# Optimization experiments

Measured on AMD Instinct MI355X. Metric: run time of the kernel, lower is better.

The kernel has to match this reference:

```python
import jax, jax.numpy as jnp
from jax import lax
import numpy as np

DN = ('NCHW', 'OIHW', 'NCHW')


def _gaussian_kernel1d(ksize, sigma):
    # torchvision GaussianBlur kernel: linspace-centered, normalized pdf
    x = jnp.linspace(-(ksize - 1) * 0.5, (ksize - 1) * 0.5, ksize, dtype=jnp.float32)
    pdf = jnp.exp(-0.5 * (x / sigma) ** 2)
    return pdf / pdf.sum()


def gaussian_blur(x, ksize, sigma):
    # x: [B, 1, H, W]. Separable blur with reflect padding (== torchvision
    # GaussianBlur, whose 2D kernel is the outer product of the 1D kernel).
    k = _gaussian_kernel1d(ksize, sigma).astype(x.dtype)
    pad = ksize // 2
    xp = jnp.pad(x, ((0, 0), (0, 0), (pad, pad), (pad, pad)), mode='reflect')
    xh = lax.conv_general_dilated(xp, k.reshape(1, 1, ksize, 1), (1, 1), 'VALID',
                                  dimension_numbers=DN)
    return lax.conv_general_dilated(xh, k.reshape(1, 1, 1, ksize), (1, 1), 'VALID',
                                    dimension_numbers=DN)


def _batch_max_norm(x):
    m = jnp.max(x.reshape(x.shape[0], -1), axis=1).reshape(-1, 1, 1, 1)
    return x / m


def _batch_mean_norm(x):
    m = jnp.mean(x.reshape(x.shape[0], -1), axis=1).reshape(-1, 1, 1, 1)
    return x / m


def setup_inputs() -> dict:
    key = jax.random.key(0)
    k1, k2, k3 = jax.random.split(key, 3)
    B, C, H, W = 8, 19, 512, 512
    mask_parse = jax.random.uniform(k1, (B, C, H, W), dtype=jnp.float32)
    area_weights = jax.random.uniform(k2, (C,), dtype=jnp.float32)
    eye_shadows_weight = jax.random.uniform(k3, (1,), dtype=jnp.float32)
    return {"mask_parse": mask_parse, "area_weights": area_weights,
            "eye_shadows_weight": eye_shadows_weight}


def reference(mask_parse, area_weights, eye_shadows_weight):
    background_mask = mask_parse[:, 0:1]          # [B,1,H,W]

    def eye_weight_mask(eyes_mask):
        w = gaussian_blur(eyes_mask, 51, 15.0)
        w = w * (1.0 - eyes_mask) * (1.0 - background_mask)
        return _batch_max_norm(w)

    w_mask_l = eye_weight_mask(mask_parse[:, 4:5])
    w_mask_r = eye_weight_mask(mask_parse[:, 5:6])

    # sum_i mask_parse[:, i] * area_weights[i]
    mask = jnp.einsum('bchw,c->bhw', mask_parse, area_weights)[:, None]
    mask = mask + (w_mask_l + w_mask_r) * eye_shadows_weight
    mask = gaussian_blur(mask, 21, 2.0)
    return _batch_mean_norm(mask)
```

## Files before the change

### kernel.cpp

```cpp
#include <hip/hip_runtime.h>
#include <hip/hip_cooperative_groups.h>

namespace cg = cooperative_groups;

constexpr int B_ = 8, C_ = 19, H_ = 512, W_ = 512;
constexpr int HW_ = H_ * W_;
constexpr int NB = 512;
constexpr int NT = 512;
constexpr int QH = 128, QW = 128;

constexpr int LDSF    = 14880;
constexpr int A_OFF   = 14336;
constexpr int SAW_OFF = 14848;
constexpr int T2Q_OFF = 2944, WHQ_OFF = 3840;
constexpr int ST_S = 540;

constexpr long WS_BM   = 0;
constexpr long WS_EW   = 512;
constexpr long WS_ESUM = 1024;
constexpr long WS_DSG  = 4096;
constexpr long WS_T0   = WS_DSG + 16L * QH * QW;

__device__ __forceinline__ int refl(int i, int n) {
    i = (i < 0) ? -i : i;
    return (i >= n) ? (2 * n - 2 - i) : i;
}

template<int ND>
__device__ __forceinline__ void gauss_reg(float (&wkr)[ND], float sigma) {
    float s = 0.f;
#pragma unroll
    for (int d = 0; d < ND; ++d) {
        const float t = d / sigma;
        wkr[d] = expf(-0.5f * t * t);
        s += (d ? 2.f : 1.f) * wkr[d];
    }
    const float inv = 1.f / s;
#pragma unroll
    for (int d = 0; d < ND; ++d) wkr[d] *= inv;
}

__device__ __forceinline__ float aweight(int i, const float (&wkr)[11]) {
    float a = 0.f;
#pragma unroll
    for (int t = 0; t < 21; ++t) {
        const float k = wkr[(t < 10) ? (10 - t) : (t - 10)];
        const int o = i + 10 - t;
        if (o >= 0 && o < H_) a += k;
        if (i >= 1 && i <= 10 && t <= 10 - i) a += k;
        if (i >= 501 && i <= 510 && t >= 521 - i) a += k;
    }
    return a;
}

__device__ __forceinline__ void ds_tile(const float* __restrict__ mp,
                                        float* __restrict__ dsg, int tid, int vb)
{
    const int b = vb >> 6, eye = (vb >> 5) & 1, ht = vb & 31;
    const int z = eye * 8 + b;
    const float* sb = mp + ((long)b * C_ + 4 + eye) * HW_;
    const int q = tid >> 7, cg = tid & 127;
    const int fr = ht * 16 + q * 4;
    float s = 0.f;
#pragma unroll
    for (int r = 0; r < 4; ++r) {
        const float4 v = *(const float4*)(sb + (long)(fr + r) * W_ + 4 * cg);
        s += (v.x + v.y) + (v.z + v.w);
    }
    dsg[(long)z * (QH * QW) + (long)(ht * 4 + q) * QW + cg] = s * 0.0625f;
}

__device__ __forceinline__ void eye_q(const float* __restrict__ mp,
                                      const float* __restrict__ dsg,
                                      float* __restrict__ t0,
                                      float* __restrict__ blockmax,
                                      float* __restrict__ eyesumw,
                                      float* lds, int tid, int vb)
{
    float kq[8];
    gauss_reg(kq, 3.75f);
    const int b = vb >> 6, eye = (vb >> 5) & 1, ht = vb & 31;
    const int z = eye * 8 + b;
    const float* dz = dsg + (long)z * (QH * QW);

    __syncthreads();
    float* sgq = lds;
    for (int t = 0; t < 6; ++t) {
        const int e = tid + t * NT;
        if (e < 20 * 142) {
            const int r = e / 142, c = e - r * 142;
            sgq[r * 142 + c] = dz[(long)refl(ht * 4 - 8 + r, QH) * QW + refl(c - 7, QW)];
        }
    }
    __syncthreads();
    float* t2q = lds + T2Q_OFF;
    if (tid < 426) {
        const int g = tid / 142, c = tid - g * 142;
        float w[16];
#pragma unroll
        for (int s = 0; s < 16; ++s) w[s] = sgq[(2 * g + s) * 142 + c];
#pragma unroll
        for (int jr = 0; jr < 2; ++jr) {
            float a = 0.f;
#pragma unroll
            for (int d = 0; d < 15; ++d)
                a = fmaf(w[jr + d], kq[(d < 7) ? (7 - d) : (d - 7)], a);
            t2q[(2 * g + jr) * 142 + c] = a;
        }
    }
    __syncthreads();
    float* whq = lds + WHQ_OFF;
#pragma unroll
    for (int t = 0; t < 2; ++t) {
        const int e = tid + t * NT;
        if (e < 768) {
            const int s = e >> 7, c = e & 127;
            float a = 0.f;
#pragma unroll
            for (int d = 0; d < 15; ++d)
                a = fmaf(t2q[s * 142 + c + d], kq[(d < 7) ? (7 - d) : (d - 7)], a);
            whq[s * 130 + c + 1] = a;
        }
    }
    __syncthreads();
    if (tid < 6) {
        whq[tid * 130]       = whq[tid * 130 + 1];
        whq[tid * 130 + 129] = whq[tid * 130 + 128];
    }
    __syncthreads();
    if (ht == 0 && tid < 130)  whq[tid]           = whq[130 + tid];
    if (ht == 31 && tid < 130) whq[5 * 130 + tid] = whq[4 * 130 + tid];
    __syncthreads();

    const float* A = lds + A_OFF;
    const int c = tid;
    const int j = ((c + 2) >> 2) - 1;
    const float fc = 0.625f + 0.25f * (float)(c & 1) - 0.5f * (float)((c >> 1) & 1);
    float cv[6];
#pragma unroll
    for (int s = 0; s < 6; ++s) {
        const float a0 = whq[s * 130 + j + 1], a1 = whq[s * 130 + j + 2];
        cv[s] = fmaf(fc, a1 - a0, a0);
    }
    const float Aw = A[c];
    const long mbase = (long)b * C_ * HW_ + (long)(ht * 16) * W_ + c;
    const float* eyp = mp + mbase + (long)(4 + eye) * HW_;
    const float* bgp = mp + mbase;
    float* db = t0 + (long)z * HW_ + (long)(ht * 16) * W_ + c;
    float vmax = 0.f, vsum = 0.f;
#pragma unroll
    for (int o = 0; o < 16; ++o) {
        const int ls0 = (o + 2) >> 2;
        const float fr_ = 0.625f + 0.25f * (float)(o & 1) - 0.5f * (float)((o >> 1) & 1);
        const float wv = fmaf(fr_, cv[ls0 + 1] - cv[ls0], cv[ls0]);
        const float ey = eyp[(long)o * W_], bg = bgp[(long)o * W_];
        const float v = wv * (1.f - ey) * (1.f - bg);
        db[(long)o * W_] = v;
        vmax = fmaxf(vmax, v);
        vsum = fmaf(v, A[ht * 16 + o] * Aw, vsum);
    }
#pragma unroll
    for (int off = 32; off; off >>= 1) {
        vmax = fmaxf(vmax, __shfl_down(vmax, off));
        vsum += __shfl_down(vsum, off);
    }
    __syncthreads();
    if ((tid & 63) == 0) { lds[tid >> 6] = vmax; lds[8 + (tid >> 6)] = vsum; }
    __syncthreads();
    if (tid == 0) {
        float m = lds[0], s = lds[8];
        for (int i = 1; i < 8; ++i) { m = fmaxf(m, lds[i]); s += lds[8 + i]; }
        blockmax[z * 32 + ht] = m;
        eyesumw[z * 32 + ht] = s;
    }
}

__device__ __forceinline__ void einsum_part(const float* __restrict__ mp,
                                            float* __restrict__ t3,
                                            float* __restrict__ esum,
                                            float* lds, int tid, int vb)
{
    const float* A   = lds + A_OFF;
    const float* saw = lds + SAW_OFF;
    const int b = vb >> 6, chunk = vb & 63;
    float se = 0.f;
#pragma unroll
    for (int q = 0; q < 2; ++q) {
        const int p4 = chunk * 1024 + q * 512 + tid;
        const long p = (long)p4 * 4;
        const int h = (int)(p >> 9), w0 = (int)(p & 511);
        const float* mpb = mp + (long)b * C_ * HW_ + p;
        float4 acc = make_float4(0.f, 0.f, 0.f, 0.f);
#pragma unroll
        for (int c = 0; c < C_; ++c) {
            const float4 v = *(const float4*)(mpb + (long)c * HW_);
            const float a = saw[c];
            acc.x = fmaf(v.x, a, acc.x);
            acc.y = fmaf(v.y, a, acc.y);
            acc.z = fmaf(v.z, a, acc.z);
            acc.w = fmaf(v.w, a, acc.w);
        }
        *(float4*)(t3 + (long)b * HW_ + p) = acc;
        const float4 a4 = *(const float4*)(A + w0);
        se = fmaf(acc.x * a4.x + acc.y * a4.y + acc.z * a4.z + acc.w * a4.w,
                  A[h], se);
    }
#pragma unroll
    for (int off = 32; off; off >>= 1) se += __shfl_down(se, off);
    __syncthreads();
    if ((tid & 63) == 0) lds[tid >> 6] = se;
    __syncthreads();
    if (tid == 0) {
        float s = 0.f;
        for (int i = 0; i < 8; ++i) s += lds[i];
        esum[vb] = s;
    }
}

__device__ __forceinline__ void phaseB(const float* __restrict__ esw,
                                       const float* __restrict__ t0,
                                       const float* __restrict__ blockmax,
                                       const float* __restrict__ eyesumw,
                                       const float* __restrict__ esum,
                                       float* __restrict__ out,
                                       float* lds, int tid, int vb)
{
    float wkr[11];
    gauss_reg(wkr, 2.f);
    const int b = vb >> 6, tile6 = vb & 63, hb = tile6 * 8;

    float mxL = blockmax[b * 32], mxR = blockmax[(8 + b) * 32];
    float SeL = 0.f, SeR = 0.f, Se = 0.f;
    for (int i = 0; i < 32; ++i) {
        mxL = fmaxf(mxL, blockmax[b * 32 + i]);
        mxR = fmaxf(mxR, blockmax[(8 + b) * 32 + i]);
        SeL += eyesumw[b * 32 + i];
        SeR += eyesumw[(8 + b) * 32 + i];
    }
    for (int i = 0; i < 64; ++i) Se += esum[b * 64 + i];
    const float e = esw[0];
    const float sl = e / mxL, sr = e / mxR;
    const float scale = (float)HW_ / (Se + sl * SeL + sr * SeR);

    const float* t1 = t0 + (long)b * HW_;
    const float* t2 = t0 + (long)(8 + b) * HW_;
    const float* t3 = t0 + (long)(16 + b) * HW_;

    const int c = tid;
    float win[28];
#pragma unroll
    for (int i = 0; i < 28; ++i) {
        const long off = (long)refl(hb - 10 + i, H_) * W_ + c;
        win[i] = fmaf(t1[off], sl, fmaf(t2[off], sr, t3[off]));
    }
    float hv[8];
#pragma unroll
    for (int j = 0; j < 8; ++j) {
        float a = 0.f;
#pragma unroll
        for (int k = 0; k < 21; ++k)
            a = fmaf(win[j + k], wkr[(k < 10) ? (10 - k) : (k - 10)], a);
        hv[j] = a;
    }
    __syncthreads();
    float* st = lds;
#pragma unroll
    for (int j = 0; j < 8; ++j) st[j * ST_S + 12 + c] = hv[j];
    __syncthreads();
    if (tid < 224) {
        const int r = tid / 28, q = tid - r * 28;
        float* srow = st + r * ST_S;
        if (q < 12) srow[11 - q] = srow[13 + q];
        else { const int cc = q - 12; srow[524 + cc] = srow[522 - cc]; }
    }
    __syncthreads();
    {
        const int r = tid >> 6, g = tid & 63, c0 = g * 8;
        const float* srow = st + r * ST_S;
        float wn[32];
#pragma unroll
        for (int m = 0; m < 8; ++m) {
            const float4 v = *(const float4*)(srow + c0 + 4 * m);
            wn[4*m] = v.x; wn[4*m+1] = v.y; wn[4*m+2] = v.z; wn[4*m+3] = v.w;
        }
        float oo[8];
#pragma unroll
        for (int o = 0; o < 8; ++o) {
            float a = 0.f;
#pragma unroll
            for (int k = 0; k < 21; ++k)
                a = fmaf(wn[o + 2 + k], wkr[(k < 10) ? (10 - k) : (k - 10)], a);
            oo[o] = a * scale;
        }
        float* orow = out + (long)b * HW_ + (long)(hb + r) * W_ + c0;
        *(float4*)(orow)     = make_float4(oo[0], oo[1], oo[2], oo[3]);
        *(float4*)(orow + 4) = make_float4(oo[4], oo[5], oo[6], oo[7]);
    }
}

__global__ void __launch_bounds__(NT, 4)
mega_kern(const float* __restrict__ mp, const float* __restrict__ aw,
          const float* __restrict__ esw, float* __restrict__ out,
          float* __restrict__ ws)
{
    cg::grid_group grid = cg::this_grid();
    __shared__ __align__(16) float lds[LDSF];
    const int tid = threadIdx.x, bid = blockIdx.x;
    const int vb = (bid & 7) * 64 + (bid >> 3);
    float* blockmax = ws + WS_BM;
    float* eyesumw  = ws + WS_EW;
    float* esum     = ws + WS_ESUM;
    float* dsg      = ws + WS_DSG;
    float* t0       = ws + WS_T0;
    float* t3       = t0 + 16L * HW_;

    {
        float w21[11];
        gauss_reg(w21, 2.f);
        lds[A_OFF + tid] = aweight(tid, w21);
    }
    if (tid < C_) lds[SAW_OFF + tid] = aw[tid];
    __syncthreads();

    ds_tile(mp, dsg, tid, vb);
    grid.sync();

    if (bid & 1) {
        einsum_part(mp, t3, esum, lds, tid, vb);
        eye_q(mp, dsg, t0, blockmax, eyesumw, lds, tid, vb);
    } else {
        eye_q(mp, dsg, t0, blockmax, eyesumw, lds, tid, vb);
        einsum_part(mp, t3, esum, lds, tid, vb);
    }
    grid.sync();

    phaseB(esw, t0, blockmax, eyesumw, esum, out, lds, tid, vb);
}

__global__ void __launch_bounds__(NT)
fb_P0_kern(const float* __restrict__ mp, float* __restrict__ ws)
{
    const int bid = blockIdx.x;
    const int vb = (bid & 7) * 64 + (bid >> 3);
    ds_tile(mp, ws + WS_DSG, threadIdx.x, vb);
}

__global__ void __launch_bounds__(NT)
fb_P1_kern(const float* __restrict__ mp, const float* __restrict__ aw,
           float* __restrict__ ws)
{
    __shared__ __align__(16) float lds[LDSF];
    const int tid = threadIdx.x, bid = blockIdx.x;
    const int vb = (bid & 7) * 64 + (bid >> 3);
    float* t0 = ws + WS_T0;
    {
        float w21[11];
        gauss_reg(w21, 2.f);
        lds[A_OFF + tid] = aweight(tid, w21);
    }
    if (tid < C_) lds[SAW_OFF + tid] = aw[tid];
    __syncthreads();
    if (bid & 1) {
        einsum_part(mp, t0 + 16L * HW_, ws + WS_ESUM, lds, tid, vb);
        eye_q(mp, ws + WS_DSG, t0, ws + WS_BM, ws + WS_EW, lds, tid, vb);
    } else {
        eye_q(mp, ws + WS_DSG, t0, ws + WS_BM, ws + WS_EW, lds, tid, vb);
        einsum_part(mp, t0 + 16L * HW_, ws + WS_ESUM, lds, tid, vb);
    }
}

__global__ void __launch_bounds__(NT)
fb_P2_kern(const float* __restrict__ esw, float* __restrict__ out,
           float* __restrict__ ws)
{
    __shared__ __align__(16) float lds[LDSF];
    const int tid = threadIdx.x, bid = blockIdx.x;
    const int vb = (bid & 7) * 64 + (bid >> 3);
    phaseB(esw, ws + WS_T0, ws + WS_BM, ws + WS_EW, ws + WS_ESUM,
           out, lds, tid, vb);
}

extern "C" void kernel_launch(void* const* d_in, const int* in_sizes, int n_in,
                              void* d_out, int out_size, void* d_ws, size_t ws_size,
                              hipStream_t stream)
{
    const float* mp  = (const float*)d_in[0];
    const float* aw  = (const float*)d_in[1];
    const float* esw = (const float*)d_in[2];
    float* out = (float*)d_out;
    float* wsf = (float*)d_ws;

    int coop = 0, nb = 0;
    hipDeviceGetAttribute(&coop, hipDeviceAttributeCooperativeLaunch, 0);
    hipOccupancyMaxActiveBlocksPerMultiprocessor(&nb, (const void*)mega_kern, NT, 0);

    if (coop && nb >= 2) {
        void* args[] = { (void*)&mp, (void*)&aw, (void*)&esw, (void*)&out, (void*)&wsf };
        hipLaunchCooperativeKernel((void*)mega_kern, dim3(NB), dim3(NT), args, 0, stream);
    } else {
        fb_P0_kern<<<NB, NT, 0, stream>>>(mp, wsf);
        fb_P1_kern<<<NB, NT, 0, stream>>>(mp, aw, wsf);
        fb_P2_kern<<<NB, NT, 0, stream>>>(esw, out, wsf);
    }
}
```

Measured before the change: 53.57 us.

## Replace cooperative mega-kernel with three regular launches and split einsum blocks

Drops the cooperative launch and its two grid-wide syncs in favour of three ordinary kernel launches on one stream. Eye work and einsum work now run in separate blocks of one mixed 1536-block launch instead of being done in sequence by each block. Per-kernel LDS is cut so more blocks can be resident, and the einsum is split into 1024 half-size chunks with a matching change in the phase-B reduction. It also removes the per-call occupancy and attribute queries on the host, at the cost of two extra kernel launch overheads.

```diff
diff --git a/kernel.cpp b/kernel.cpp
--- a/kernel.cpp
+++ b/kernel.cpp
@@ -1,18 +1,12 @@
 #include <hip/hip_runtime.h>
-#include <hip/hip_cooperative_groups.h>
-
-namespace cg = cooperative_groups;
 
 constexpr int B_ = 8, C_ = 19, H_ = 512, W_ = 512;
 constexpr int HW_ = H_ * W_;
-constexpr int NB = 512;
 constexpr int NT = 512;
 constexpr int QH = 128, QW = 128;
 
-constexpr int LDSF    = 14880;
-constexpr int A_OFF   = 14336;
-constexpr int SAW_OFF = 14848;
-constexpr int T2Q_OFF = 2944, WHQ_OFF = 3840;
+constexpr int T2Q_OFF = 2944, WHQ_OFF = 3840, A_OFF = 4640, SAW_OFF = 5152;
+constexpr int K1_LDSF = 5184;
 constexpr int ST_S = 540;
 
 constexpr long WS_BM   = 0;
@@ -53,9 +47,12 @@
     return a;
 }
 
-__device__ __forceinline__ void ds_tile(const float* __restrict__ mp,
-                                        float* __restrict__ dsg, int tid, int vb)
-{
+__global__ void __launch_bounds__(NT)
+k0_ds(const float* __restrict__ mp, float* __restrict__ ws)
+{
+    float* dsg = ws + WS_DSG;
+    const int bid = blockIdx.x, tid = threadIdx.x;
+    const int vb = (bid & 7) * 64 + (bid >> 3);
     const int b = vb >> 6, eye = (vb >> 5) & 1, ht = vb & 31;
     const int z = eye * 8 + b;
     const float* sb = mp + ((long)b * C_ + 4 + eye) * HW_;
@@ -83,7 +80,6 @@
     const int z = eye * 8 + b;
     const float* dz = dsg + (long)z * (QH * QW);
 
-    __syncthreads();
     float* sgq = lds;
     for (int t = 0; t < 6; ++t) {
         const int e = tid + t * NT;
@@ -175,36 +171,31 @@
     }
 }
 
-__device__ __forceinline__ void einsum_part(const float* __restrict__ mp,
+__device__ __forceinline__ void einsum_half(const float* __restrict__ mp,
                                             float* __restrict__ t3,
                                             float* __restrict__ esum,
-                                            float* lds, int tid, int vb)
+                                            float* lds, int tid, int idx)
 {
     const float* A   = lds + A_OFF;
     const float* saw = lds + SAW_OFF;
-    const int b = vb >> 6, chunk = vb & 63;
-    float se = 0.f;
-#pragma unroll
-    for (int q = 0; q < 2; ++q) {
-        const int p4 = chunk * 1024 + q * 512 + tid;
-        const long p = (long)p4 * 4;
-        const int h = (int)(p >> 9), w0 = (int)(p & 511);
-        const float* mpb = mp + (long)b * C_ * HW_ + p;
-        float4 acc = make_float4(0.f, 0.f, 0.f, 0.f);
-#pragma unroll
-        for (int c = 0; c < C_; ++c) {
-            const float4 v = *(const float4*)(mpb + (long)c * HW_);
-            const float a = saw[c];
-            acc.x = fmaf(v.x, a, acc.x);
-            acc.y = fmaf(v.y, a, acc.y);
-            acc.z = fmaf(v.z, a, acc.z);
-            acc.w = fmaf(v.w, a, acc.w);
-        }
-        *(float4*)(t3 + (long)b * HW_ + p) = acc;
-        const float4 a4 = *(const float4*)(A + w0);
-        se = fmaf(acc.x * a4.x + acc.y * a4.y + acc.z * a4.z + acc.w * a4.w,
-                  A[h], se);
-    }
+    const int b = idx >> 7, ch = idx & 127;
+    const int p4 = ch * 512 + tid;
+    const long p = (long)p4 * 4;
+    const int h = (int)(p >> 9), w0 = (int)(p & 511);
+    const float* mpb = mp + (long)b * C_ * HW_ + p;
+    float4 acc = make_float4(0.f, 0.f, 0.f, 0.f);
+#pragma unroll
+    for (int c = 0; c < C_; ++c) {
+        const float4 v = *(const float4*)(mpb + (long)c * HW_);
+        const float a = saw[c];
+        acc.x = fmaf(v.x, a, acc.x);
+        acc.y = fmaf(v.y, a, acc.y);
+        acc.z = fmaf(v.z, a, acc.z);
+        acc.w = fmaf(v.w, a, acc.w);
+    }
+    *(float4*)(t3 + (long)b * HW_ + p) = acc;
+    const float4 a4 = *(const float4*)(A + w0);
+    float se = (acc.x * a4.x + acc.y * a4.y + acc.z * a4.z + acc.w * a4.w) * A[h];
 #pragma unroll
     for (int off = 32; off; off >>= 1) se += __shfl_down(se, off);
     __syncthreads();
@@ -213,18 +204,53 @@
     if (tid == 0) {
         float s = 0.f;
         for (int i = 0; i < 8; ++i) s += lds[i];
-        esum[vb] = s;
-    }
-}
-
-__device__ __forceinline__ void phaseB(const float* __restrict__ esw,
-                                       const float* __restrict__ t0,
-                                       const float* __restrict__ blockmax,
-                                       const float* __restrict__ eyesumw,
-                                       const float* __restrict__ esum,
-                                       float* __restrict__ out,
-                                       float* lds, int tid, int vb)
-{
+        esum[idx] = s;
+    }
+}
+
+__global__ void __launch_bounds__(NT, 8)
+k1_mix(const float* __restrict__ mp, const float* __restrict__ aw,
+       float* __restrict__ ws)
+{
+    __shared__ __align__(16) float lds[K1_LDSF];
+    const int tid = threadIdx.x, bid = blockIdx.x;
+    float* blockmax = ws + WS_BM;
+    float* eyesumw  = ws + WS_EW;
+    float* esum     = ws + WS_ESUM;
+    float* dsg      = ws + WS_DSG;
+    float* t0       = ws + WS_T0;
+    float* t3       = t0 + 16L * HW_;
+
+    {
+        float w21[11];
+        gauss_reg(w21, 2.f);
+        lds[A_OFF + tid] = aweight(tid, w21);
+    }
+    if (tid < C_) lds[SAW_OFF + tid] = aw[tid];
+    __syncthreads();
+
+    if (bid < 512) {
+        const int vb = (bid & 7) * 64 + (bid >> 3);
+        eye_q(mp, dsg, t0, blockmax, eyesumw, lds, tid, vb);
+    } else {
+        const int raw = bid - 512;
+        const int idx = (raw & 7) * 128 + (raw >> 3);
+        einsum_half(mp, t3, esum, lds, tid, idx);
+    }
+}
+
+__global__ void __launch_bounds__(NT, 4)
+k2_blur(const float* __restrict__ esw, float* __restrict__ out,
+        float* __restrict__ ws)
+{
+    __shared__ __align__(16) float lds[ST_S * 8 + 32];
+    const int tid = threadIdx.x, bid = blockIdx.x;
+    const int vb = (bid & 7) * 64 + (bid >> 3);
+    const float* blockmax = ws + WS_BM;
+    const float* eyesumw  = ws + WS_EW;
+    const float* esum     = ws + WS_ESUM;
+    const float* t0       = ws + WS_T0;
+
     float wkr[11];
     gauss_reg(wkr, 2.f);
     const int b = vb >> 6, tile6 = vb & 63, hb = tile6 * 8;
@@ -237,7 +263,7 @@
         SeL += eyesumw[b * 32 + i];
         SeR += eyesumw[(8 + b) * 32 + i];
     }
-    for (int i = 0; i < 64; ++i) Se += esum[b * 64 + i];
+    for (int i = 0; i < 128; ++i) Se += esum[b * 128 + i];
     const float e = esw[0];
     const float sl = e / mxL, sr = e / mxR;
     const float scale = (float)HW_ / (Se + sl * SeL + sr * SeR);
@@ -262,7 +288,6 @@
             a = fmaf(win[j + k], wkr[(k < 10) ? (10 - k) : (k - 10)], a);
         hv[j] = a;
     }
-    __syncthreads();
     float* st = lds;
 #pragma unroll
     for (int j = 0; j < 8; ++j) st[j * ST_S + 12 + c] = hv[j];
@@ -298,88 +323,6 @@
     }
 }
 
-__global__ void __launch_bounds__(NT, 4)
-mega_kern(const float* __restrict__ mp, const float* __restrict__ aw,
-          const float* __restrict__ esw, float* __restrict__ out,
-          float* __restrict__ ws)
-{
-    cg::grid_group grid = cg::this_grid();
-    __shared__ __align__(16) float lds[LDSF];
-    const int tid = threadIdx.x, bid = blockIdx.x;
-    const int vb = (bid & 7) * 64 + (bid >> 3);
-    float* blockmax = ws + WS_BM;
-    float* eyesumw  = ws + WS_EW;
-    float* esum     = ws + WS_ESUM;
-    float* dsg      = ws + WS_DSG;
-    float* t0       = ws + WS_T0;
-    float* t3       = t0 + 16L * HW_;
-
-    {
-        float w21[11];
-        gauss_reg(w21, 2.f);
-        lds[A_OFF + tid] = aweight(tid, w21);
-    }
-    if (tid < C_) lds[SAW_OFF + tid] = aw[tid];
-    __syncthreads();
-
-    ds_tile(mp, dsg, tid, vb);
-    grid.sync();
-
-    if (bid & 1) {
-        einsum_part(mp, t3, esum, lds, tid, vb);
-        eye_q(mp, dsg, t0, blockmax, eyesumw, lds, tid, vb);
-    } else {
-        eye_q(mp, dsg, t0, blockmax, eyesumw, lds, tid, vb);
-        einsum_part(mp, t3, esum, lds, tid, vb);
-    }
-    grid.sync();
-
-    phaseB(esw, t0, blockmax, eyesumw, esum, out, lds, tid, vb);
-}
-
-__global__ void __launch_bounds__(NT)
-fb_P0_kern(const float* __restrict__ mp, float* __restrict__ ws)
-{
-    const int bid = blockIdx.x;
-    const int vb = (bid & 7) * 64 + (bid >> 3);
-    ds_tile(mp, ws + WS_DSG, threadIdx.x, vb);
-}
-
-__global__ void __launch_bounds__(NT)
-fb_P1_kern(const float* __restrict__ mp, const float* __restrict__ aw,
-           float* __restrict__ ws)
-{
-    __shared__ __align__(16) float lds[LDSF];
-    const int tid = threadIdx.x, bid = blockIdx.x;
-    const int vb = (bid & 7) * 64 + (bid >> 3);
-    float* t0 = ws + WS_T0;
-    {
-        float w21[11];
-        gauss_reg(w21, 2.f);
-        lds[A_OFF + tid] = aweight(tid, w21);
-    }
-    if (tid < C_) lds[SAW_OFF + tid] = aw[tid];
-    __syncthreads();
-    if (bid & 1) {
-        einsum_part(mp, t0 + 16L * HW_, ws + WS_ESUM, lds, tid, vb);
-        eye_q(mp, ws + WS_DSG, t0, ws + WS_BM, ws + WS_EW, lds, tid, vb);
-    } else {
-        eye_q(mp, ws + WS_DSG, t0, ws + WS_BM, ws + WS_EW, lds, tid, vb);
-        einsum_part(mp, t0 + 16L * HW_, ws + WS_ESUM, lds, tid, vb);
-    }
-}
-
-__global__ void __launch_bounds__(NT)
-fb_P2_kern(const float* __restrict__ esw, float* __restrict__ out,
-           float* __restrict__ ws)
-{
-    __shared__ __align__(16) float lds[LDSF];
-    const int tid = threadIdx.x, bid = blockIdx.x;
-    const int vb = (bid & 7) * 64 + (bid >> 3);
-    phaseB(esw, ws + WS_T0, ws + WS_BM, ws + WS_EW, ws + WS_ESUM,
-           out, lds, tid, vb);
-}
-
 extern "C" void kernel_launch(void* const* d_in, const int* in_sizes, int n_in,
                               void* d_out, int out_size, void* d_ws, size_t ws_size,
                               hipStream_t stream)
@@ -390,16 +333,7 @@
     float* out = (float*)d_out;
     float* wsf = (float*)d_ws;
 
-    int coop = 0, nb = 0;
-    hipDeviceGetAttribute(&coop, hipDeviceAttributeCooperativeLaunch, 0);
-    hipOccupancyMaxActiveBlocksPerMultiprocessor(&nb, (const void*)mega_kern, NT, 0);
-
-    if (coop && nb >= 2) {
-        void* args[] = { (void*)&mp, (void*)&aw, (void*)&esw, (void*)&out, (void*)&wsf };
-        hipLaunchCooperativeKernel((void*)mega_kern, dim3(NB), dim3(NT), args, 0, stream);
-    } else {
-        fb_P0_kern<<<NB, NT, 0, stream>>>(mp, wsf);
-        fb_P1_kern<<<NB, NT, 0, stream>>>(mp, aw, wsf);
-        fb_P2_kern<<<NB, NT, 0, stream>>>(esw, out, wsf);
-    }
-}
+    k0_ds  <<<512,  NT, 0, stream>>>(mp, wsf);
+    k1_mix <<<1536, NT, 0, stream>>>(mp, aw, wsf);
+    k2_blur<<<512,  NT, 0, stream>>>(esw, out, wsf);
+}
```

Result: no change. 54.46 us (+1.7%).

## Split downsample into separate kernel and replace grid syncs with per-batch counters

Applied to the files above, without the earlier changes.

The downsample stage moves into its own preceding kernel, which also zeroes the per-batch completion counters. The first grid-wide barrier is replaced by the kernel boundary, and the second by a per-batch atomic counter spin-wait, so each batch's 64 blocks proceed to the final blur without waiting on the whole grid. The LDS footprint is also trimmed so more blocks can be resident. This adds an extra launch and relies on all 64 blocks of a batch being co-resident for the spin-wait, which the cooperative launch provides.

```diff
diff --git a/kernel.cpp b/kernel.cpp
--- a/kernel.cpp
+++ b/kernel.cpp
@@ -9,15 +9,14 @@
 constexpr int NT = 512;
 constexpr int QH = 128, QW = 128;
 
-constexpr int LDSF    = 14880;
-constexpr int A_OFF   = 14336;
-constexpr int SAW_OFF = 14848;
-constexpr int T2Q_OFF = 2944, WHQ_OFF = 3840;
+constexpr int T2Q_OFF = 2944, WHQ_OFF = 3840, A_OFF = 4640, SAW_OFF = 5152;
+constexpr int LDSF = 5184;
 constexpr int ST_S = 540;
 
 constexpr long WS_BM   = 0;
 constexpr long WS_EW   = 512;
 constexpr long WS_ESUM = 1024;
+constexpr long WS_DONE = 2048;
 constexpr long WS_DSG  = 4096;
 constexpr long WS_T0   = WS_DSG + 16L * QH * QW;
 
@@ -53,9 +52,13 @@
     return a;
 }
 
-__device__ __forceinline__ void ds_tile(const float* __restrict__ mp,
-                                        float* __restrict__ dsg, int tid, int vb)
-{
+__global__ void __launch_bounds__(NT)
+k0_ds(const float* __restrict__ mp, float* __restrict__ ws)
+{
+    float* dsg = ws + WS_DSG;
+    const int bid = blockIdx.x, tid = threadIdx.x;
+    if (bid == 0 && tid < 8) ((unsigned int*)(ws + WS_DONE))[tid] = 0u;
+    const int vb = (bid & 7) * 64 + (bid >> 3);
     const int b = vb >> 6, eye = (vb >> 5) & 1, ht = vb & 31;
     const int z = eye * 8 + b;
     const float* sb = mp + ((long)b * C_ + 4 + eye) * HW_;
@@ -75,15 +78,14 @@
                                       float* __restrict__ t0,
                                       float* __restrict__ blockmax,
                                       float* __restrict__ eyesumw,
-                                      float* lds, int tid, int vb)
+                                      float* lds, int tid, int b, int slot)
 {
     float kq[8];
     gauss_reg(kq, 3.75f);
-    const int b = vb >> 6, eye = (vb >> 5) & 1, ht = vb & 31;
+    const int eye = slot >> 5, ht = slot & 31;
     const int z = eye * 8 + b;
     const float* dz = dsg + (long)z * (QH * QW);
 
-    __syncthreads();
     float* sgq = lds;
     for (int t = 0; t < 6; ++t) {
         const int e = tid + t * NT;
@@ -178,15 +180,14 @@
 __device__ __forceinline__ void einsum_part(const float* __restrict__ mp,
                                             float* __restrict__ t3,
                                             float* __restrict__ esum,
-                                            float* lds, int tid, int vb)
+                                            float* lds, int tid, int b, int slot)
 {
     const float* A   = lds + A_OFF;
     const float* saw = lds + SAW_OFF;
-    const int b = vb >> 6, chunk = vb & 63;
     float se = 0.f;
 #pragma unroll
     for (int q = 0; q < 2; ++q) {
-        const int p4 = chunk * 1024 + q * 512 + tid;
+        const int p4 = slot * 1024 + q * 512 + tid;
         const long p = (long)p4 * 4;
         const int h = (int)(p >> 9), w0 = (int)(p & 511);
         const float* mpb = mp + (long)b * C_ * HW_ + p;
@@ -213,7 +214,7 @@
     if (tid == 0) {
         float s = 0.f;
         for (int i = 0; i < 8; ++i) s += lds[i];
-        esum[vb] = s;
+        esum[b * 64 + slot] = s;
     }
 }
 
@@ -223,11 +224,11 @@
                                        const float* __restrict__ eyesumw,
                                        const float* __restrict__ esum,
                                        float* __restrict__ out,
-                                       float* lds, int tid, int vb)
+                                       float* lds, int tid, int b, int slot)
 {
     float wkr[11];
     gauss_reg(wkr, 2.f);
-    const int b = vb >> 6, tile6 = vb & 63, hb = tile6 * 8;
+    const int hb = slot * 8;
 
     float mxL = blockmax[b * 32], mxR = blockmax[(8 + b) * 32];
     float SeL = 0.f, SeR = 0.f, Se = 0.f;
@@ -262,7 +263,6 @@
             a = fmaf(win[j + k], wkr[(k < 10) ? (10 - k) : (k - 10)], a);
         hv[j] = a;
     }
-    __syncthreads();
     float* st = lds;
 #pragma unroll
     for (int j = 0; j < 8; ++j) st[j * ST_S + 12 + c] = hv[j];
@@ -299,17 +299,18 @@
 }
 
 __global__ void __launch_bounds__(NT, 4)
-mega_kern(const float* __restrict__ mp, const float* __restrict__ aw,
-          const float* __restrict__ esw, float* __restrict__ out,
-          float* __restrict__ ws)
-{
-    cg::grid_group grid = cg::this_grid();
+k1_mega(const float* __restrict__ mp, const float* __restrict__ aw,
+        const float* __restrict__ esw, float* __restrict__ out,
+        float* __restrict__ ws)
+{
     __shared__ __align__(16) float lds[LDSF];
     const int tid = threadIdx.x, bid = blockIdx.x;
-    const int vb = (bid & 7) * 64 + (bid >> 3);
+    const int b = bid & 7;
+    const int slot = bid >> 3;
     float* blockmax = ws + WS_BM;
     float* eyesumw  = ws + WS_EW;
     float* esum     = ws + WS_ESUM;
+    unsigned int* done = (unsigned int*)(ws + WS_DONE);
     float* dsg      = ws + WS_DSG;
     float* t0       = ws + WS_T0;
     float* t3       = t0 + 16L * HW_;
@@ -322,36 +323,35 @@
     if (tid < C_) lds[SAW_OFF + tid] = aw[tid];
     __syncthreads();
 
-    ds_tile(mp, dsg, tid, vb);
-    grid.sync();
-
     if (bid & 1) {
-        einsum_part(mp, t3, esum, lds, tid, vb);
-        eye_q(mp, dsg, t0, blockmax, eyesumw, lds, tid, vb);
+        einsum_part(mp, t3, esum, lds, tid, b, slot);
+        __syncthreads();
+        eye_q(mp, dsg, t0, blockmax, eyesumw, lds, tid, b, slot);
     } else {
-        eye_q(mp, dsg, t0, blockmax, eyesumw, lds, tid, vb);
-        einsum_part(mp, t3, esum, lds, tid, vb);
-    }
-    grid.sync();
-
-    phaseB(esw, t0, blockmax, eyesumw, esum, out, lds, tid, vb);
+        eye_q(mp, dsg, t0, blockmax, eyesumw, lds, tid, b, slot);
+        __syncthreads();
+        einsum_part(mp, t3, esum, lds, tid, b, slot);
+    }
+
+    __syncthreads();
+    if (tid == 0) {
+        __threadfence();
+        atomicAdd(&done[b], 1u);
+        while (atomicAdd(&done[b], 0u) < 64u) __builtin_amdgcn_s_sleep(8);
+    }
+    __syncthreads();
+    __threadfence();
+
+    phaseB(esw, t0, blockmax, eyesumw, esum, out, lds, tid, b, slot);
 }
 
 __global__ void __launch_bounds__(NT)
-fb_P0_kern(const float* __restrict__ mp, float* __restrict__ ws)
-{
-    const int bid = blockIdx.x;
-    const int vb = (bid & 7) * 64 + (bid >> 3);
-    ds_tile(mp, ws + WS_DSG, threadIdx.x, vb);
-}
-
-__global__ void __launch_bounds__(NT)
-fb_P1_kern(const float* __restrict__ mp, const float* __restrict__ aw,
-           float* __restrict__ ws)
+fb_A_kern(const float* __restrict__ mp, const float* __restrict__ aw,
+          float* __restrict__ ws)
 {
     __shared__ __align__(16) float lds[LDSF];
     const int tid = threadIdx.x, bid = blockIdx.x;
-    const int vb = (bid & 7) * 64 + (bid >> 3);
+    const int b = bid & 7, slot = bid >> 3;
     float* t0 = ws + WS_T0;
     {
         float w21[11];
@@ -361,23 +361,24 @@
     if (tid < C_) lds[SAW_OFF + tid] = aw[tid];
     __syncthreads();
     if (bid & 1) {
-        einsum_part(mp, t0 + 16L * HW_, ws + WS_ESUM, lds, tid, vb);
-        eye_q(mp, ws + WS_DSG, t0, ws + WS_BM, ws + WS_EW, lds, tid, vb);
+        einsum_part(mp, t0 + 16L * HW_, ws + WS_ESUM, lds, tid, b, slot);
+        __syncthreads();
+        eye_q(mp, ws + WS_DSG, t0, ws + WS_BM, ws + WS_EW, lds, tid, b, slot);
     } else {
-        eye_q(mp, ws + WS_DSG, t0, ws + WS_BM, ws + WS_EW, lds, tid, vb);
-        einsum_part(mp, t0 + 16L * HW_, ws + WS_ESUM, lds, tid, vb);
+        eye_q(mp, ws + WS_DSG, t0, ws + WS_BM, ws + WS_EW, lds, tid, b, slot);
+        __syncthreads();
+        einsum_part(mp, t0 + 16L * HW_, ws + WS_ESUM, lds, tid, b, slot);
     }
 }
 
 __global__ void __launch_bounds__(NT)
-fb_P2_kern(const float* __restrict__ esw, float* __restrict__ out,
-           float* __restrict__ ws)
+fb_B_kern(const float* __restrict__ esw, float* __restrict__ out,
+          float* __restrict__ ws)
 {
     __shared__ __align__(16) float lds[LDSF];
     const int tid = threadIdx.x, bid = blockIdx.x;
-    const int vb = (bid & 7) * 64 + (bid >> 3);
     phaseB(esw, ws + WS_T0, ws + WS_BM, ws + WS_EW, ws + WS_ESUM,
-           out, lds, tid, vb);
+           out, lds, tid, bid & 7, bid >> 3);
 }
 
 extern "C" void kernel_launch(void* const* d_in, const int* in_sizes, int n_in,
@@ -390,16 +391,17 @@
     float* out = (float*)d_out;
     float* wsf = (float*)d_ws;
 
+    k0_ds<<<NB, NT, 0, stream>>>(mp, wsf);
+
     int coop = 0, nb = 0;
     hipDeviceGetAttribute(&coop, hipDeviceAttributeCooperativeLaunch, 0);
-    hipOccupancyMaxActiveBlocksPerMultiprocessor(&nb, (const void*)mega_kern, NT, 0);
+    hipOccupancyMaxActiveBlocksPerMultiprocessor(&nb, (const void*)k1_mega, NT, 0);
 
     if (coop && nb >= 2) {
         void* args[] = { (void*)&mp, (void*)&aw, (void*)&esw, (void*)&out, (void*)&wsf };
-        hipLaunchCooperativeKernel((void*)mega_kern, dim3(NB), dim3(NT), args, 0, stream);
+        hipLaunchCooperativeKernel((void*)k1_mega, dim3(NB), dim3(NT), args, 0, stream);
     } else {
-        fb_P0_kern<<<NB, NT, 0, stream>>>(mp, wsf);
-        fb_P1_kern<<<NB, NT, 0, stream>>>(mp, aw, wsf);
-        fb_P2_kern<<<NB, NT, 0, stream>>>(esw, out, wsf);
-    }
-}
+        fb_A_kern<<<NB, NT, 0, stream>>>(mp, aw, wsf);
+        fb_B_kern<<<NB, NT, 0, stream>>>(esw, out, wsf);
+    }
+}
```

New measurement: 55.02 us. 2.7% more time.
